# Optimization experiments

Measured on AMD Instinct MI355X. Metric: run time of the kernel, lower is better.

## Reference

```python
import jax, jax.numpy as jnp
import numpy as np

DIM = 1024
HEADS = 16
HIDDEN = 4 * DIM


def layernorm(x, g, b, eps=1e-5):
    mu = jnp.mean(x, axis=-1, keepdims=True)
    var = jnp.mean(jnp.square(x - mu), axis=-1, keepdims=True)
    return (x - mu) * jax.lax.rsqrt(var + eps) * g + b


def setup_inputs() -> dict:
    key = jax.random.key(0)
    ks = jax.random.split(key, 8)
    s = DIM ** -0.5
    return {
        "x": jax.random.normal(ks[0], (2, 2048, DIM), dtype=jnp.float32),
        "ln1_g": jnp.ones((DIM,), jnp.float32),
        "ln1_b": jnp.zeros((DIM,), jnp.float32),
        "qkv_w": jax.random.normal(ks[1], (DIM, 3 * DIM), jnp.float32) * s,
        "proj_w": jax.random.normal(ks[2], (DIM, DIM), jnp.float32) * s,
        "proj_b": jnp.zeros((DIM,), jnp.float32),
        "ln2_g": jnp.ones((DIM,), jnp.float32),
        "ln2_b": jnp.zeros((DIM,), jnp.float32),
        "fc1_w": jax.random.normal(ks[3], (DIM, HIDDEN), jnp.float32) * s,
        "fc1_b": jnp.zeros((HIDDEN,), jnp.float32),
        "fc2_w": jax.random.normal(ks[4], (HIDDEN, DIM), jnp.float32) * (HIDDEN ** -0.5),
        "fc2_b": jnp.zeros((DIM,), jnp.float32),
    }


def block_fwd(x, ln1_g, ln1_b, qkv_w, proj_w, proj_b, ln2_g, ln2_b,
              fc1_w, fc1_b, fc2_w, fc2_b):
    B, N, C = x.shape
    H = HEADS
    Dh = C // H
    scale = Dh ** -0.5
    # --- attention branch (pre-norm) ---
    h = layernorm(x, ln1_g, ln1_b)
    qkv = h @ qkv_w                     # [B,N,3C] (no bias: qkv_bias=False)
    qkv = qkv.reshape(B, N, 3, H, Dh)
    q = qkv[:, :, 0].transpose(0, 2, 1, 3)   # [B,H,N,Dh]
    k = qkv[:, :, 1].transpose(0, 2, 1, 3)
    v = qkv[:, :, 2].transpose(0, 2, 1, 3)
    attn = jnp.einsum('bhqd,bhkd->bhqk', q, k) * scale
    attn = jax.nn.softmax(attn, axis=-1)
    o = jnp.einsum('bhqk,bhkd->bhqd', attn, v)
    o = o.transpose(0, 2, 1, 3).reshape(B, N, C)
    x = x + (o @ proj_w + proj_b)
    # --- MLP branch (pre-norm) ---
    h = layernorm(x, ln2_g, ln2_b)
    h = jax.nn.gelu(h @ fc1_w + fc1_b, approximate=False)  # torch nn.GELU = exact erf
    x = x + (h @ fc2_w + fc2_b)
    return x


def reference(x, ln1_g, ln1_b, qkv_w, proj_w, proj_b, ln2_g, ln2_b,
              fc1_w, fc1_b, fc2_w, fc2_b):
    return block_fwd(x, ln1_g, ln1_b, qkv_w, proj_w, proj_b, ln2_g, ln2_b,
                     fc1_w, fc1_b, fc2_w, fc2_b)
```

## Files before the change

### kernel.cpp

```cpp
#include <hip/hip_runtime.h>
#include <math.h>

typedef unsigned short u16;
typedef unsigned int u32;
typedef __attribute__((ext_vector_type(8))) short short8;
typedef __attribute__((ext_vector_type(4))) float f32x4;
typedef __attribute__((ext_vector_type(16))) float f32x16;
typedef __attribute__((ext_vector_type(2))) u32 u32x2;
typedef __attribute__((ext_vector_type(4))) u32 u32x4;
typedef __attribute__((ext_vector_type(4))) u16 u16x4;

typedef __attribute__((address_space(1))) const void gmem_t;
typedef __attribute__((address_space(3))) void lmem_t;

__device__ __forceinline__ u16 f2bf(float f) {
  u32 u = __builtin_bit_cast(u32, f);
  u = u + 0x7fffu + ((u >> 16) & 1u);
  return (u16)(u >> 16);
}

__device__ __forceinline__ u32 cvt_pk_bf16(float a, float b) {
  u32 r;
  asm("v_cvt_pk_bf16_f32 %0, %1, %2" : "=v"(r) : "v"(a), "v"(b));
  return r;
}

__device__ __forceinline__ void g2l16(const void* g, void* l) {
  __builtin_amdgcn_global_load_lds((gmem_t*)g, (lmem_t*)l, 16, 0, 0);
}

template <int N> __device__ __forceinline__ void waitcnt_vm() {
  if constexpr (N == 0)      asm volatile("s_waitcnt vmcnt(0)" ::: "memory");
  else if constexpr (N == 4) asm volatile("s_waitcnt vmcnt(4)" ::: "memory");
  else if constexpr (N == 6) asm volatile("s_waitcnt vmcnt(6)" ::: "memory");
  else if constexpr (N == 8) asm volatile("s_waitcnt vmcnt(8)" ::: "memory");
  else static_assert(N == 0 || N == 4 || N == 6 || N == 8, "add literal");
}

__global__ __launch_bounds__(256) void wtrans_all(
    const float* __restrict__ qkvw, const float* __restrict__ projw,
    const float* __restrict__ fc1w, const float* __restrict__ fc2w,
    u16* __restrict__ o_qkv, u16* __restrict__ o_proj,
    u16* __restrict__ o_fc1, u16* __restrict__ o_fc2) {
  int id = (int)blockIdx.x;
  const float* in; u16* out; int R, C, bid;
  if (id < 768)       { in = qkvw;  out = o_qkv;  R = 1024; C = 3072; bid = id; }
  else if (id < 1024) { in = projw; out = o_proj; R = 1024; C = 1024; bid = id - 768; }
  else if (id < 2048) { in = fc1w;  out = o_fc1;  R = 1024; C = 4096; bid = id - 1024; }
  else                { in = fc2w;  out = o_fc2;  R = 4096; C = 1024; bid = id - 2048; }
  __shared__ float t[64][65];
  int tid = threadIdx.x;
  int nbx = C >> 6;
  int bx = bid % nbx, by = bid / nbx;
  int r0 = by << 6, c0 = bx << 6;
  int lr = tid >> 2, lc = (tid & 3) << 4;
  const float* src = in + (size_t)(r0 + lr) * C + c0 + lc;
#pragma unroll
  for (int j = 0; j < 4; ++j) {
    f32x4 v = *(const f32x4*)(src + j * 4);
    t[lr][lc + j * 4 + 0] = v.x; t[lr][lc + j * 4 + 1] = v.y;
    t[lr][lc + j * 4 + 2] = v.z; t[lr][lc + j * 4 + 3] = v.w;
  }
  __syncthreads();
  int oc = tid >> 2, orr = (tid & 3) << 4;
  u16* dst = out + (size_t)(c0 + oc) * R + r0 + orr;
  u32 u[8];
#pragma unroll
  for (int j = 0; j < 8; ++j)
    u[j] = (u32)f2bf(t[orr + 2 * j][oc]) | ((u32)f2bf(t[orr + 2 * j + 1][oc]) << 16);
  u32x4 v0; v0.x = u[0]; v0.y = u[1]; v0.z = u[2]; v0.w = u[3];
  u32x4 v1; v1.x = u[4]; v1.y = u[5]; v1.z = u[6]; v1.w = u[7];
  *(u32x4*)(dst) = v0;
  *(u32x4*)(dst + 8) = v1;
}

__global__ __launch_bounds__(256) void lnorm(const float* __restrict__ in,
                                             const float* __restrict__ gw,
                                             const float* __restrict__ bw,
                                             u16* __restrict__ out) {
  int r = blockIdx.x, tid = threadIdx.x;
  const f32x4 v = *((const f32x4*)(in + (size_t)r * 1024) + tid);
  float s = v.x + v.y + v.z + v.w;
  float ss = v.x * v.x + v.y * v.y + v.z * v.z + v.w * v.w;
#pragma unroll
  for (int o = 32; o >= 1; o >>= 1) { s += __shfl_xor(s, o); ss += __shfl_xor(ss, o); }
  __shared__ float red[8];
  int w = tid >> 6;
  if ((tid & 63) == 0) { red[w] = s; red[4 + w] = ss; }
  __syncthreads();
  s = red[0] + red[1] + red[2] + red[3];
  ss = red[4] + red[5] + red[6] + red[7];
  float mu = s * (1.0f / 1024.0f);
  float var = ss * (1.0f / 1024.0f) - mu * mu;
  float rstd = rsqrtf(var + 1e-5f);
  const f32x4 g4 = *((const f32x4*)gw + tid);
  const f32x4 b4 = *((const f32x4*)bw + tid);
  u16x4 o;
  o.x = f2bf((v.x - mu) * rstd * g4.x + b4.x);
  o.y = f2bf((v.y - mu) * rstd * g4.y + b4.y);
  o.z = f2bf((v.z - mu) * rstd * g4.z + b4.z);
  o.w = f2bf((v.w - mu) * rstd * g4.w + b4.w);
  *((u16x4*)(out + (size_t)r * 1024) + tid) = o;
}

template <int EPI, int BM, int BN>
__global__ __launch_bounds__(256, 2) void gemm_bt(
    const u16* __restrict__ A, const u16* __restrict__ BT, int M, int N, int K,
    const float* __restrict__ bias, const float* __restrict__ resid,
    float* __restrict__ fout, u16* __restrict__ bout,
    u16* __restrict__ bout2, u16* __restrict__ bout3) {
  constexpr int AIT = BM / 32, BIT = BN / 32;
  constexpr int L = AIT + BIT;
  constexpr int MR = BM / 32, NR = BN / 32;
  __shared__ __align__(16) u16 smA[2][BM * 64];
  __shared__ __align__(16) u16 smB[2][BN * 64];
  int tid = threadIdx.x;
  int w = tid >> 6, l = tid & 63, lq = l & 15, g = l >> 4;
  int nbx = N / BN;
  int t = (int)blockIdx.x;
  int cpx = (int)gridDim.x >> 3;
  t = (t & 7) * cpx + (t >> 3);
  int by = t / nbx, bx = t - by * nbx;
  long brow = (long)by * BM, bcol = (long)bx * BN;
  int wr = w >> 1, wc = w & 1;

  const u16* aS[AIT]; const u16* bS[BIT];
#pragma unroll
  for (int it = 0; it < AIT; ++it) {
    int p = it * 256 + tid;
    int row = p >> 3;
    int gc = (p & 7) ^ (row & 7);
    aS[it] = A + (size_t)(brow + row) * K + gc * 8;
  }
#pragma unroll
  for (int it = 0; it < BIT; ++it) {
    int p = it * 256 + tid;
    int row = p >> 3;
    int gc = (p & 7) ^ (row & 7);
    bS[it] = BT + (size_t)(bcol + row) * K + gc * 8;
  }
  auto STAGE = [&](int buf, int k0) {
#pragma unroll
    for (int it = 0; it < AIT; ++it) g2l16(aS[it] + k0, &smA[buf][it * 2048 + w * 512]);
#pragma unroll
    for (int it = 0; it < BIT; ++it) g2l16(bS[it] + k0, &smB[buf][it * 2048 + w * 512]);
  };

  f32x4 zero = {0.f, 0.f, 0.f, 0.f};
  f32x4 acc[MR][NR];
#pragma unroll
  for (int m = 0; m < MR; ++m)
#pragma unroll
    for (int n = 0; n < NR; ++n) acc[m][n] = zero;

  int NT = K >> 6;
  STAGE(0, 0);
  for (int tt = 0; tt < NT; ++tt) {
    int cur = tt & 1;
    int knext = ((tt + 1) == NT ? 0 : (tt + 1)) << 6;
    STAGE(cur ^ 1, knext);
    waitcnt_vm<L>();
    __builtin_amdgcn_s_barrier();
    asm volatile("" ::: "memory");

    const char* sA = (const char*)&smA[cur][0];
    const char* sB = (const char*)&smB[cur][0];
#pragma unroll
    for (int c = 0; c < 2; ++c) {
      short8 af[MR], bfb[NR];
#pragma unroll
      for (int m = 0; m < MR; ++m) {
        int r = wr * (BM / 2) + m * 16 + lq;
        af[m] = *(const short8*)(sA + r * 128 + ((g * 16 + c * 64) ^ ((r & 7) << 4)));
      }
#pragma unroll
      for (int n = 0; n < NR; ++n) {
        int r = wc * (BN / 2) + n * 16 + lq;
        bfb[n] = *(const short8*)(sB + r * 128 + ((g * 16 + c * 64) ^ ((r & 7) << 4)));
      }
#pragma unroll
      for (int m = 0; m < MR; ++m)
#pragma unroll
        for (int n = 0; n < NR; ++n)
          acc[m][n] = __builtin_amdgcn_mfma_f32_16x16x32_bf16(af[m], bfb[n], acc[m][n], 0, 0, 0);
    }
    asm volatile("" ::: "memory");
    __builtin_amdgcn_s_barrier();
  }
  waitcnt_vm<0>();

  long colbase = bcol + wc * (BN / 2);
#pragma unroll
  for (int m = 0; m < MR; ++m) {
#pragma unroll
    for (int n = 0; n < NR; ++n) {
      f32x4 v = acc[m][n];
      long col = colbase + n * 16 + lq;
      long row0 = brow + wr * (BM / 2) + m * 16 + g * 4;
      if constexpr (EPI == 0) {
        int part = (int)(bcol >> 10);
        long colq = col - ((long)part << 10);
        int hh = (int)(colq >> 6), d = (int)(colq & 63);
#pragma unroll
        for (int i = 0; i < 4; ++i) {
          long row = row0 + i;
          long b = row >> 11, nq = row & 2047;
          long bh = b * 16 + hh;
          u16 val = f2bf(v[i]);
          if (part == 0)      bout [(bh * 2048 + nq) * 64 + d] = val;
          else if (part == 1) bout2[(bh * 2048 + nq) * 64 + d] = val;
          else                bout3[(bh * 64 + d) * 2048 + nq] = val;
        }
      } else if constexpr (EPI == 1 || EPI == 3) {
        float bb = bias[col];
#pragma unroll
        for (int i = 0; i < 4; ++i) {
          long idx = (row0 + i) * N + col;
          fout[idx] = resid[idx] + v[i] + bb;
        }
      } else {
        float bb = bias[col];
#pragma unroll
        for (int i = 0; i < 4; ++i) {
          float xg = v[i] + bb;
          float ge = 0.5f * xg * (1.0f + erff(xg * 0.70710678118654752f));
          bout[(row0 + i) * N + col] = f2bf(ge);
        }
      }
    }
  }
}

template <int BASE>
__device__ __forceinline__ short8 mk_pfrag(const f32x16& s, float sc) {
  u32 x = cvt_pk_bf16(exp2f(s[BASE + 0] * sc - 12.0f), exp2f(s[BASE + 1] * sc - 12.0f));
  u32 y = cvt_pk_bf16(exp2f(s[BASE + 2] * sc - 12.0f), exp2f(s[BASE + 3] * sc - 12.0f));
  u32 u = cvt_pk_bf16(exp2f(s[BASE + 4] * sc - 12.0f), exp2f(s[BASE + 5] * sc - 12.0f));
  u32 v = cvt_pk_bf16(exp2f(s[BASE + 6] * sc - 12.0f), exp2f(s[BASE + 7] * sc - 12.0f));
  asm("v_permlane32_swap_b32 %0, %1" : "+v"(x), "+v"(u));
  asm("v_permlane32_swap_b32 %0, %1" : "+v"(y), "+v"(v));
  u32x4 f; f.x = x; f.y = y; f.z = u; f.w = v;
  return __builtin_bit_cast(short8, f);
}

__global__ __launch_bounds__(256, 2) void attn_fwd(const u16* __restrict__ qb,
                                                   const u16* __restrict__ kbuf,
                                                   const u16* __restrict__ vtb,
                                                   u16* __restrict__ ob) {
  __shared__ __align__(16) u16 kl[2][64 * 64];
  __shared__ __align__(16) u16 vl[2][64 * 64];
  int tid = threadIdx.x;
  int w = tid >> 6, l = tid & 63, q32 = l & 31, hi = l >> 5;
  int bh = (int)blockIdx.x & 31;
  int qt = (int)blockIdx.x >> 5;

  const u16* qp = qb + ((size_t)bh * 2048 + qt * 128 + w * 32 + q32) * 64 + hi * 8;
  short8 qf[4];
#pragma unroll
  for (int kc = 0; kc < 4; ++kc) qf[kc] = *(const short8*)(qp + kc * 16);

  const u16* kS[2]; const u16* vS[2];
#pragma unroll
  for (int it = 0; it < 2; ++it) {
    int p = it * 256 + tid;
    int row = p >> 3;
    int gc = (p & 7) ^ (row & 7);
    kS[it] = kbuf + ((size_t)bh * 2048 + row) * 64 + gc * 8;
    vS[it] = vtb + ((size_t)bh * 64 + row) * 2048 + gc * 8;
  }
  auto issue = [&](int buf, int kt0) {
#pragma unroll
    for (int it = 0; it < 2; ++it) {
      g2l16(kS[it] + (size_t)kt0 * 64, &kl[buf][it * 2048 + w * 512]);
      g2l16(vS[it] + kt0,              &vl[buf][it * 2048 + w * 512]);
    }
  };

  f32x16 z16 = {0,0,0,0,0,0,0,0,0,0,0,0,0,0,0,0};
  f32x16 accO0 = z16, accO1 = z16, accl = z16;
  const float sc = 0.125f * 1.44269504088896f;
  u32x4 ov; ov.x = ov.y = ov.z = ov.w = 0x3F803F80u;
  short8 onesf = __builtin_bit_cast(short8, ov);
  int swz = (q32 & 7) << 4;

  issue(0, 0);
  for (int t = 0; t < 32; ++t) {
    int cur = t & 1;
    issue(cur ^ 1, ((t + 1) & 31) << 6);
    waitcnt_vm<4>();
    __builtin_amdgcn_s_barrier();
    asm volatile("" ::: "memory");

    const char* klc = (const char*)&kl[cur][0];
    const char* vlc = (const char*)&vl[cur][0];

    f32x16 s0 = z16, s1 = z16;
    __builtin_amdgcn_s_setprio(1);
#pragma unroll
    for (int kc = 0; kc < 4; ++kc) {
      short8 k0 = *(const short8*)(klc + (q32 * 128 +        ((kc * 32 + hi * 16) ^ swz)));
      short8 k1 = *(const short8*)(klc + ((32 + q32) * 128 + ((kc * 32 + hi * 16) ^ swz)));
      s0 = __builtin_amdgcn_mfma_f32_32x32x16_bf16(k0, qf[kc], s0, 0, 0, 0);
      s1 = __builtin_amdgcn_mfma_f32_32x32x16_bf16(k1, qf[kc], s1, 0, 0, 0);
    }
    __builtin_amdgcn_s_setprio(0);

    short8 pf0 = mk_pfrag<0>(s0, sc);
    short8 pf1 = mk_pfrag<8>(s0, sc);
    short8 pf2 = mk_pfrag<0>(s1, sc);
    short8 pf3 = mk_pfrag<8>(s1, sc);

    short8 va0[4], va1[4];
#pragma unroll
    for (int c = 0; c < 4; ++c) {
      va0[c] = *(const short8*)(vlc + (q32 * 128 +        ((c * 32 + hi * 16) ^ swz)));
      va1[c] = *(const short8*)(vlc + ((32 + q32) * 128 + ((c * 32 + hi * 16) ^ swz)));
    }
    __builtin_amdgcn_s_setprio(1);
    accO0 = __builtin_amdgcn_mfma_f32_32x32x16_bf16(va0[0], pf0, accO0, 0, 0, 0);
    accO1 = __builtin_amdgcn_mfma_f32_32x32x16_bf16(va1[0], pf0, accO1, 0, 0, 0);
    accl  = __builtin_amdgcn_mfma_f32_32x32x16_bf16(onesf,  pf0, accl,  0, 0, 0);
    accO0 = __builtin_amdgcn_mfma_f32_32x32x16_bf16(va0[1], pf1, accO0, 0, 0, 0);
    accO1 = __builtin_amdgcn_mfma_f32_32x32x16_bf16(va1[1], pf1, accO1, 0, 0, 0);
    accl  = __builtin_amdgcn_mfma_f32_32x32x16_bf16(onesf,  pf1, accl,  0, 0, 0);
    accO0 = __builtin_amdgcn_mfma_f32_32x32x16_bf16(va0[2], pf2, accO0, 0, 0, 0);
    accO1 = __builtin_amdgcn_mfma_f32_32x32x16_bf16(va1[2], pf2, accO1, 0, 0, 0);
    accl  = __builtin_amdgcn_mfma_f32_32x32x16_bf16(onesf,  pf2, accl,  0, 0, 0);
    accO0 = __builtin_amdgcn_mfma_f32_32x32x16_bf16(va0[3], pf3, accO0, 0, 0, 0);
    accO1 = __builtin_amdgcn_mfma_f32_32x32x16_bf16(va1[3], pf3, accO1, 0, 0, 0);
    accl  = __builtin_amdgcn_mfma_f32_32x32x16_bf16(onesf,  pf3, accl,  0, 0, 0);
    __builtin_amdgcn_s_setprio(0);

    asm volatile("" ::: "memory");
    __builtin_amdgcn_s_barrier();
  }
  waitcnt_vm<0>();

  float li = 1.0f / accl[0];
  int b = bh >> 4, h = bh & 15;
  long q = (long)qt * 128 + w * 32 + q32;
  u16* obase = ob + ((long)b * 2048 + q) * 1024 + h * 64;
#pragma unroll
  for (int j = 0; j < 8; ++j) {
    int d = ((2 * j) & 3) + 8 * (j >> 1) + 4 * hi;
    *(u32*)(obase + d)      = cvt_pk_bf16(accO0[2 * j] * li, accO0[2 * j + 1] * li);
    *(u32*)(obase + 32 + d) = cvt_pk_bf16(accO1[2 * j] * li, accO1[2 * j + 1] * li);
  }
}

extern "C" void kernel_launch(void* const* d_in, const int* in_sizes, int n_in,
                              void* d_out, int out_size, void* d_ws, size_t ws_size,
                              hipStream_t stream) {
  const float* x     = (const float*)d_in[0];
  const float* ln1g  = (const float*)d_in[1];
  const float* ln1b  = (const float*)d_in[2];
  const float* qkvw  = (const float*)d_in[3];
  const float* projw = (const float*)d_in[4];
  const float* projb = (const float*)d_in[5];
  const float* ln2g  = (const float*)d_in[6];
  const float* ln2b  = (const float*)d_in[7];
  const float* fc1w  = (const float*)d_in[8];
  const float* fc1b  = (const float*)d_in[9];
  const float* fc2w  = (const float*)d_in[10];
  const float* fc2b  = (const float*)d_in[11];
  char* ws = (char*)d_ws;
  u16* qkv_wt  = (u16*)(ws + 0);
  u16* proj_wt = (u16*)(ws + 6291456);
  u16* fc1_wt  = (u16*)(ws + 8388608);
  u16* fc2_wt  = (u16*)(ws + 16777216);
  u16* h       = (u16*)(ws + 25165824);
  u16* qbuf    = (u16*)(ws + 33554432);
  u16* kbuf    = (u16*)(ws + 41943040);
  u16* vtbuf   = (u16*)(ws + 50331648);
  u16* aout    = (u16*)(ws + 58720256);
  float* y1    = (float*)(ws + 67108864);
  u16* gbuf    = (u16*)(ws + 33554432);
  float* outp  = (float*)d_out;

  wtrans_all<<<3072, 256, 0, stream>>>(qkvw, projw, fc1w, fc2w,
                                       qkv_wt, proj_wt, fc1_wt, fc2_wt);

  lnorm<<<4096, 256, 0, stream>>>(x, ln1g, ln1b, h);
  gemm_bt<0, 128, 128><<<768, 256, 0, stream>>>(h, qkv_wt, 4096, 3072, 1024,
                                      nullptr, nullptr, nullptr, qbuf, kbuf, vtbuf);
  attn_fwd<<<512, 256, 0, stream>>>(qbuf, kbuf, vtbuf, aout);
  gemm_bt<1, 64, 128><<<512, 256, 0, stream>>>(aout, proj_wt, 4096, 1024, 1024,
                                      projb, x, y1, nullptr, nullptr, nullptr);
  lnorm<<<4096, 256, 0, stream>>>(y1, ln2g, ln2b, h);
  gemm_bt<2, 128, 128><<<1024, 256, 0, stream>>>(h, fc1_wt, 4096, 4096, 1024,
                                       fc1b, nullptr, nullptr, gbuf, nullptr, nullptr);
  gemm_bt<3, 64, 128><<<512, 256, 0, stream>>>(gbuf, fc2_wt, 4096, 1024, 4096,
                                      fc2b, y1, outp, nullptr, nullptr, nullptr);
}
```

Measured before the change: 263.5 us.

## Use 256x256-tile 512-thread GEMM for QKV and FC1 projections

```diff
diff --git a/kernel.cpp b/kernel.cpp
--- a/kernel.cpp
+++ b/kernel.cpp
@@ -107,8 +107,7 @@
 __global__ __launch_bounds__(256, 2) void gemm_bt(
     const u16* __restrict__ A, const u16* __restrict__ BT, int M, int N, int K,
     const float* __restrict__ bias, const float* __restrict__ resid,
-    float* __restrict__ fout, u16* __restrict__ bout,
-    u16* __restrict__ bout2, u16* __restrict__ bout3) {
+    float* __restrict__ fout, u16* __restrict__ bout) {
   constexpr int AIT = BM / 32, BIT = BN / 32;
   constexpr int L = AIT + BIT;
   constexpr int MR = BM / 32, NR = BN / 32;
@@ -197,34 +196,129 @@
       f32x4 v = acc[m][n];
       long col = colbase + n * 16 + lq;
       long row0 = brow + wr * (BM / 2) + m * 16 + g * 4;
-      if constexpr (EPI == 0) {
-        int part = (int)(bcol >> 10);
-        long colq = col - ((long)part << 10);
-        int hh = (int)(colq >> 6), d = (int)(colq & 63);
-#pragma unroll
-        for (int i = 0; i < 4; ++i) {
-          long row = row0 + i;
-          long b = row >> 11, nq = row & 2047;
-          long bh = b * 16 + hh;
-          u16 val = f2bf(v[i]);
-          if (part == 0)      bout [(bh * 2048 + nq) * 64 + d] = val;
-          else if (part == 1) bout2[(bh * 2048 + nq) * 64 + d] = val;
-          else                bout3[(bh * 64 + d) * 2048 + nq] = val;
-        }
-      } else if constexpr (EPI == 1 || EPI == 3) {
-        float bb = bias[col];
-#pragma unroll
-        for (int i = 0; i < 4; ++i) {
-          long idx = (row0 + i) * N + col;
-          fout[idx] = resid[idx] + v[i] + bb;
-        }
-      } else {
-        float bb = bias[col];
-#pragma unroll
-        for (int i = 0; i < 4; ++i) {
-          float xg = v[i] + bb;
-          float ge = 0.5f * xg * (1.0f + erff(xg * 0.70710678118654752f));
-          bout[(row0 + i) * N + col] = f2bf(ge);
+      float bb = bias[col];
+#pragma unroll
+      for (int i = 0; i < 4; ++i) {
+        long idx = (row0 + i) * N + col;
+        fout[idx] = resid[idx] + v[i] + bb;
+      }
+    }
+  }
+}
+
+template <int EPI>
+__global__ __launch_bounds__(512, 2) void gemm_big(
+    const u16* __restrict__ A, const u16* __restrict__ BT, int M, int N, int K,
+    const float* __restrict__ bias,
+    u16* __restrict__ bout, u16* __restrict__ bout2, u16* __restrict__ bout3) {
+  __shared__ __align__(16) u16 smA[2][256 * 32];
+  __shared__ __align__(16) u16 smB[2][256 * 32];
+  int tid = threadIdx.x;
+  int w = tid >> 6, l = tid & 63, lq = l & 15, g = l >> 4;
+  int nbx = N >> 8;
+  int t = (int)blockIdx.x;
+  int cpx = (int)gridDim.x >> 3;
+  t = (t & 7) * cpx + (t >> 3);
+  int by = t / nbx, bx = t - by * nbx;
+  long brow = (long)by << 8, bcol = (long)bx << 8;
+  int wr = w >> 2, wc = w & 3;
+
+  const u16* aS[2]; const u16* bS[2];
+#pragma unroll
+  for (int it = 0; it < 2; ++it) {
+    int p = it * 512 + tid;
+    int row = p >> 2;
+    int gc = (p & 3) ^ (row & 3);
+    aS[it] = A + (size_t)(brow + row) * K + gc * 8;
+    bS[it] = BT + (size_t)(bcol + row) * K + gc * 8;
+  }
+  auto STAGE = [&](int buf, int k0) {
+#pragma unroll
+    for (int it = 0; it < 2; ++it) {
+      g2l16(aS[it] + k0, &smA[buf][it * 4096 + w * 512]);
+      g2l16(bS[it] + k0, &smB[buf][it * 4096 + w * 512]);
+    }
+  };
+
+  f32x4 zero = {0.f, 0.f, 0.f, 0.f};
+  f32x4 acc[2][4][4];
+#pragma unroll
+  for (int h = 0; h < 2; ++h)
+#pragma unroll
+    for (int m = 0; m < 4; ++m)
+#pragma unroll
+      for (int n = 0; n < 4; ++n) acc[h][m][n] = zero;
+
+  int NT = K >> 5;
+  STAGE(0, 0);
+  for (int tt = 0; tt < NT; ++tt) {
+    int cur = tt & 1;
+    int knext = ((tt + 1) == NT ? 0 : (tt + 1)) << 5;
+    STAGE(cur ^ 1, knext);
+    waitcnt_vm<4>();
+    __builtin_amdgcn_s_barrier();
+    asm volatile("" ::: "memory");
+
+    const char* sA = (const char*)&smA[cur][0];
+    const char* sB = (const char*)&smB[cur][0];
+    short8 bfb[4];
+#pragma unroll
+    for (int n = 0; n < 4; ++n) {
+      int r = wc * 64 + n * 16 + lq;
+      bfb[n] = *(const short8*)(sB + r * 64 + ((g * 16) ^ ((r & 3) << 4)));
+    }
+#pragma unroll
+    for (int h = 0; h < 2; ++h) {
+      short8 af[4];
+#pragma unroll
+      for (int m = 0; m < 4; ++m) {
+        int r = wr * 128 + h * 64 + m * 16 + lq;
+        af[m] = *(const short8*)(sA + r * 64 + ((g * 16) ^ ((r & 3) << 4)));
+      }
+      __builtin_amdgcn_s_setprio(1);
+#pragma unroll
+      for (int m = 0; m < 4; ++m)
+#pragma unroll
+        for (int n = 0; n < 4; ++n)
+          acc[h][m][n] = __builtin_amdgcn_mfma_f32_16x16x32_bf16(af[m], bfb[n], acc[h][m][n], 0, 0, 0);
+      __builtin_amdgcn_s_setprio(0);
+    }
+    asm volatile("" ::: "memory");
+    __builtin_amdgcn_s_barrier();
+  }
+  waitcnt_vm<0>();
+
+#pragma unroll
+  for (int h = 0; h < 2; ++h) {
+#pragma unroll
+    for (int m = 0; m < 4; ++m) {
+#pragma unroll
+      for (int n = 0; n < 4; ++n) {
+        f32x4 v = acc[h][m][n];
+        long col = bcol + wc * 64 + n * 16 + lq;
+        long row0 = brow + wr * 128 + h * 64 + m * 16 + g * 4;
+        if constexpr (EPI == 0) {
+          int part = (int)(bcol >> 10);
+          long colq = col - ((long)part << 10);
+          int hh = (int)(colq >> 6), d = (int)(colq & 63);
+#pragma unroll
+          for (int i = 0; i < 4; ++i) {
+            long row = row0 + i;
+            long b = row >> 11, nq = row & 2047;
+            long bh = b * 16 + hh;
+            u16 val = f2bf(v[i]);
+            if (part == 0)      bout [(bh * 2048 + nq) * 64 + d] = val;
+            else if (part == 1) bout2[(bh * 2048 + nq) * 64 + d] = val;
+            else                bout3[(bh * 64 + d) * 2048 + nq] = val;
+          }
+        } else {
+          float bb = bias[col];
+#pragma unroll
+          for (int i = 0; i < 4; ++i) {
+            float xg = v[i] + bb;
+            float ge = 0.5f * xg * (1.0f + erff(xg * 0.70710678118654752f));
+            bout[(row0 + i) * (long)N + col] = f2bf(ge);
+          }
         }
       }
     }
@@ -381,14 +475,14 @@
                                        qkv_wt, proj_wt, fc1_wt, fc2_wt);
 
   lnorm<<<4096, 256, 0, stream>>>(x, ln1g, ln1b, h);
-  gemm_bt<0, 128, 128><<<768, 256, 0, stream>>>(h, qkv_wt, 4096, 3072, 1024,
-                                      nullptr, nullptr, nullptr, qbuf, kbuf, vtbuf);
+  gemm_big<0><<<192, 512, 0, stream>>>(h, qkv_wt, 4096, 3072, 1024,
+                                       nullptr, qbuf, kbuf, vtbuf);
   attn_fwd<<<512, 256, 0, stream>>>(qbuf, kbuf, vtbuf, aout);
   gemm_bt<1, 64, 128><<<512, 256, 0, stream>>>(aout, proj_wt, 4096, 1024, 1024,
-                                      projb, x, y1, nullptr, nullptr, nullptr);
+                                               projb, x, y1, nullptr);
   lnorm<<<4096, 256, 0, stream>>>(y1, ln2g, ln2b, h);
-  gemm_bt<2, 128, 128><<<1024, 256, 0, stream>>>(h, fc1_wt, 4096, 4096, 1024,
-                                       fc1b, nullptr, nullptr, gbuf, nullptr, nullptr);
+  gemm_big<2><<<256, 512, 0, stream>>>(h, fc1_wt, 4096, 4096, 1024,
+                                       fc1b, gbuf, nullptr, nullptr);
   gemm_bt<3, 64, 128><<<512, 256, 0, stream>>>(gbuf, fc2_wt, 4096, 1024, 4096,
-                                      fc2b, y1, outp, nullptr, nullptr, nullptr);
-}
+                                               fc2b, y1, outp, nullptr);
+}
```

Result: slower. 282.7 us (+7.3%).
